# Kernel tuning notes

Hardware: AMD Instinct MI355X
Metric: run time of the kernel (lower is better)

The kernel has to match this reference:

```python
import jax, jax.numpy as jnp
import numpy as np

K = 3          # kernel_size
STRIDE = 1
PAD = 1
DIL = 1


def setup_inputs() -> dict:
    key = jax.random.key(0)
    k1, k2, k3, k4, k5 = jax.random.split(key, 5)
    x = jax.random.normal(k1, (4, 64, 128, 128), jnp.float32)
    weight = jax.random.normal(k2, (64, 64, K, K), jnp.float32) * 0.05   # [O, C, K, K]
    bias = jax.random.normal(k3, (64,), jnp.float32) * 0.05
    # offset conv params: small nonzero so offsets actually exercise bilinear sampling
    offset_w = jax.random.normal(k4, (2 * K * K, 64, K, K), jnp.float32) * 0.01
    offset_b = jax.random.normal(k5, (2 * K * K,), jnp.float32) * 0.1
    return {"x": x, "weight": weight, "bias": bias,
            "offset_w": offset_w, "offset_b": offset_b}


def _conv2d(x, w, b):
    y = jax.lax.conv_general_dilated(
        x, w, window_strides=(STRIDE, STRIDE),
        padding=((PAD, PAD), (PAD, PAD)), rhs_dilation=(DIL, DIL),
        dimension_numbers=("NCHW", "OIHW", "NCHW"))
    return y + b[None, :, None, None]


def _bilinear_sample(img, ys, xs):
    # img: [C, H, W]; ys, xs: [KK, Ho, Wo] float sampling coords
    H, W = img.shape[1], img.shape[2]
    y0 = jnp.floor(ys)
    x0 = jnp.floor(xs)
    y1 = y0 + 1.0
    x1 = x0 + 1.0
    wy1 = ys - y0
    wx1 = xs - x0
    wy0 = 1.0 - wy1
    wx0 = 1.0 - wx1

    def gather(yy, xx):
        valid = (yy >= 0) & (yy <= H - 1) & (xx >= 0) & (xx <= W - 1)
        yi = jnp.clip(yy, 0, H - 1).astype(jnp.int32)
        xi = jnp.clip(xx, 0, W - 1).astype(jnp.int32)
        v = img[:, yi, xi]                     # [C, KK, Ho, Wo]
        return v * valid.astype(img.dtype)

    return (gather(y0, x0) * (wy0 * wx0) + gather(y0, x1) * (wy0 * wx1)
            + gather(y1, x0) * (wy1 * wx0) + gather(y1, x1) * (wy1 * wx1))


def reference(x, weight, bias, offset_w, offset_b):
    B, C, H, W = x.shape
    KK = K * K
    # offsets: [B, 2*K*K, Ho, Wo], per-location (dy, dx) for each kernel tap
    offset = _conv2d(x, offset_w, offset_b)
    Ho, Wo = offset.shape[2], offset.shape[3]
    off = offset.reshape(B, KK, 2, Ho, Wo)
    dy, dx = off[:, :, 0], off[:, :, 1]        # [B, KK, Ho, Wo]

    ki, kj = jnp.meshgrid(jnp.arange(K), jnp.arange(K), indexing="ij")
    ki = ki.reshape(KK).astype(x.dtype)
    kj = kj.reshape(KK).astype(x.dtype)
    oy = (jnp.arange(Ho) * STRIDE - PAD).astype(x.dtype)
    ox = (jnp.arange(Wo) * STRIDE - PAD).astype(x.dtype)
    base_y = oy[None, :, None] + (ki * DIL)[:, None, None]   # [KK, Ho, 1]
    base_x = ox[None, None, :] + (kj * DIL)[:, None, None]   # [KK, 1, Wo]
    ys = base_y[None] + dy                                   # [B, KK, Ho, Wo]
    xs = base_x[None] + dx

    # sampled: [B, C, KK, Ho, Wo]
    sampled = jax.vmap(_bilinear_sample)(x, ys, xs)
    w = weight.reshape(weight.shape[0], C, KK)
    out = jnp.einsum("bckhw,ock->bohw", sampled, w) + bias[None, :, None, None]
    return out
```

## Files before the change

### kernel.cpp

```cpp
#include <hip/hip_runtime.h>
#include <hip/hip_bf16.h>

#define B_ 4
#define C_ 64
#define H_ 128
#define W_ 128
#define HW_ (H_ * W_)
#define OCH_ 18

typedef __attribute__((ext_vector_type(8))) short short8;
typedef __attribute__((ext_vector_type(16))) float f32x16;
typedef __attribute__((ext_vector_type(2))) float float2v;

#define W2B_ELEMS (9 * 2 * 4 * 64 * 8)
#define W2A_ELEMS (36 * 64 * 8)

#define PSTRIDE_B (6 * 128 * 16 + 16)
#define WIN_BYTES (8 * PSTRIDE_B)
#define OFFL_OFS  WIN_BYTES
#define OFFW_B    (OCH_ * 32 * 4)
#define SMEM_BYTES (WIN_BYTES + 8 * OFFW_B)

__device__ __forceinline__ unsigned short f2bf(float f) {
  union { float f; unsigned u; } v; v.f = f;
  unsigned r = v.u + 0x7FFFu + ((v.u >> 16) & 1u);
  return (unsigned short)(r >> 16);
}
__device__ __forceinline__ float bf2f(unsigned short h) {
  union { unsigned u; float f; } v; v.u = ((unsigned)h) << 16;
  return v.f;
}
__device__ __forceinline__ unsigned short f2bfh(float f) {
  __hip_bfloat16 h = __float2bfloat16(f);
  return *reinterpret_cast<unsigned short*>(&h);
}
__device__ __forceinline__ float uaf(unsigned u) {
  union { unsigned u; float f; } v; v.u = u; return v.f;
}
__device__ __forceinline__ int swz256(int x) { return (x & 7) * 32 + (x >> 3); }

__global__ __launch_bounds__(256) void pack_w_only(
    const float* __restrict__ wmain, const float* __restrict__ offw,
    unsigned short* __restrict__ ws_u) {
  int idx = blockIdx.x * 256 + threadIdx.x;
  if (idx < W2B_ELEMS) {
    int i = idx & 7, lane = (idx >> 3) & 63, s = (idx >> 9) & 3;
    int mq = (idx >> 11) & 1, t = idx >> 12;
    int o = mq * 32 + (lane & 31);
    int c = 16 * s + (lane >> 5) * 8 + i;
    ws_u[idx] = f2bf(wmain[(o * 64 + c) * 9 + t]);
  } else if (idx < W2B_ELEMS + W2A_ELEMS) {
    int j = idx - W2B_ELEMS;
    int i = j & 7, lane = (j >> 3) & 63, s = j >> 9;
    int kg = 16 * s + (lane >> 5) * 8 + i;
    int t = kg >> 6, c = kg & 63, oc = lane & 31;
    ws_u[idx] = (oc < OCH_) ? f2bf(offw[(oc * 64 + c) * 9 + t]) : (unsigned short)0;
  }
}

__global__ __launch_bounds__(512, 2) void deform_fused8(
    const float* __restrict__ x, const float* __restrict__ bias,
    const float* __restrict__ ob, const unsigned short* __restrict__ w2b,
    const unsigned short* __restrict__ w2a, float* __restrict__ out) {
  const int blk = swz256(blockIdx.x);
  const int ho0 = (blk & 63) * 2;
  const int b   = blk >> 6;
  const int tid = threadIdx.x;
  const int lane = tid & 63;
  const int wave = tid >> 6;
  const int r_off = wave >> 2;
  const int pair  = wave & 3;
  const int ho = ho0 + r_off;
  const int pxl = lane & 31;
  const int px = pair * 32 + pxl;
  const int laneh = lane >> 5;

  __shared__ __align__(16) char smem[SMEM_BYTES];

  const float* xb = x + (size_t)b * C_ * HW_;
  #pragma unroll
  for (int it = 0; it < 3; ++it) {
    const int u = tid + it * 512;
    const int row  = u >> 8;
    const int p    = (u >> 5) & 7;
    const int col4 = u & 31;
    const int srow = min(H_ - 1, max(0, ho0 - 2 + row));
    const float* bp = xb + (size_t)(p * 8) * HW_ + srow * W_ + col4 * 4;
    float4 f[8];
    #pragma unroll
    for (int i = 0; i < 8; ++i) f[i] = *(const float4*)(bp + (size_t)i * HW_);
    char* outb = smem + p * PSTRIDE_B + (((row << 7) + col4 * 4) << 4);
    #pragma unroll
    for (int j = 0; j < 4; ++j) {
      short8 v;
      #pragma unroll
      for (int i = 0; i < 8; ++i)
        v[i] = (short)f2bfh(reinterpret_cast<const float*>(&f[i])[j]);
      *(short8*)(outb + j * 16) = v;
    }
  }
  __syncthreads();

  f32x16 pacc_a, pacc_b;
  #pragma unroll
  for (int r = 0; r < 16; ++r) { pacc_a[r] = 0.f; pacc_b[r] = 0.f; }

  #pragma unroll 1
  for (int sq = 0; sq < 18; ++sq) {
    #pragma unroll
    for (int h = 0; h < 2; ++h) {
      const int s = 2 * sq + h;
      const int t = s >> 2;
      const int ki = (t >= 6) ? 2 : ((t >= 3) ? 1 : 0);
      const int kj = t - 3 * ki;
      const int row = ho - 1 + ki;
      const int col = px - 1 + kj;
      short8 bfr = {0, 0, 0, 0, 0, 0, 0, 0};
      if (((unsigned)row < (unsigned)H_) && ((unsigned)col < (unsigned)W_))
        bfr = *(const short8*)(smem + ((s & 3) * 2 + laneh) * PSTRIDE_B
                               + ((((ki + 1 + r_off) << 7) + col) << 4));
      const short8 afr = *(const short8*)&w2a[((size_t)s * 64 + lane) * 8];
      if (h)
        pacc_b = __builtin_amdgcn_mfma_f32_32x32x16_bf16(afr, bfr, pacc_b, 0, 0, 0);
      else
        pacc_a = __builtin_amdgcn_mfma_f32_32x32x16_bf16(afr, bfr, pacc_a, 0, 0, 0);
    }
  }

  float* offl = (float*)(smem + OFFL_OFS + wave * OFFW_B);
  #pragma unroll
  for (int reg = 0; reg < 16; ++reg) {
    const int oc = (reg & 3) + 8 * (reg >> 2) + 4 * laneh;
    if (oc < OCH_) offl[oc * 32 + pxl] = pacc_a[reg] + pacc_b[reg] + ob[oc];
  }

  f32x16 acc0, acc1;
  #pragma unroll
  for (int r = 0; r < 16; ++r) { acc0[r] = 0.f; acc1[r] = 0.f; }

  #pragma unroll 1
  for (int t = 0; t < 9; ++t) {
    const int ki = (t >= 6) ? 2 : ((t >= 3) ? 1 : 0);
    const int kj = t - 3 * ki;
    const float dy = offl[(2 * t) * 32 + pxl];
    const float dx = offl[(2 * t + 1) * 32 + pxl];
    const float ys = (float)(ho - 1 + ki) + dy;
    const float xs = (float)(px - 1 + kj) + dx;
    const float y0f = floorf(ys), x0f = floorf(xs);
    const int y0 = (int)y0f, x0 = (int)x0f;
    const int y1 = y0 + 1, x1 = x0 + 1;
    const float wy1 = ys - y0f, wx1 = xs - x0f;
    const float wy0 = 1.f - wy1, wx0 = 1.f - wx1;
    const bool vy0 = (unsigned)y0 < (unsigned)H_, vy1 = (unsigned)y1 < (unsigned)H_;
    const bool vx0 = (unsigned)x0 < (unsigned)W_, vx1 = (unsigned)x1 < (unsigned)W_;
    const float g00 = (vy0 && vx0) ? wy0 * wx0 : 0.f;
    const float g01 = (vy0 && vx1) ? wy0 * wx1 : 0.f;
    const float g10 = (vy1 && vx0) ? wy1 * wx0 : 0.f;
    const float g11 = (vy1 && vx1) ? wy1 * wx1 : 0.f;
    const int yc0 = min(max(y0, 0), H_ - 1), yc1 = min(max(y1, 0), H_ - 1);
    const int xc0 = min(max(x0, 0), W_ - 1), xc1 = min(max(x1, 0), W_ - 1);
    const int rr0 = yc0 - ho0 + 2, rr1 = yc1 - ho0 + 2;
    const bool in = ((unsigned)rr0 < 6u) & ((unsigned)rr1 < 6u);
    const unsigned short* wt2 = w2b + t * 4096;

    if (__builtin_expect(__any(!in), 0)) {
      #pragma unroll 1
      for (int ss = 0; ss < 4; ++ss) {
        short8 bf;
        #pragma unroll
        for (int i = 0; i < 8; ++i) {
          const float* img = xb + (size_t)((2 * ss + laneh) * 8 + i) * HW_;
          float v = g00 * img[yc0 * W_ + xc0] + g01 * img[yc0 * W_ + xc1]
                  + g10 * img[yc1 * W_ + xc0] + g11 * img[yc1 * W_ + xc1];
          bf[i] = (short)f2bfh(v);
        }
        const short8 a0 = *(const short8*)&wt2[(ss * 64 + lane) * 8];
        const short8 a1 = *(const short8*)&wt2[((4 + ss) * 64 + lane) * 8];
        acc0 = __builtin_amdgcn_mfma_f32_32x32x16_bf16(a0, bf, acc0, 0, 0, 0);
        acc1 = __builtin_amdgcn_mfma_f32_32x32x16_bf16(a1, bf, acc1, 0, 0, 0);
      }
      continue;
    }

    const int u00 = ((rr0 << 7) + xc0) << 4, u01 = ((rr0 << 7) + xc1) << 4;
    const int u10 = ((rr1 << 7) + xc0) << 4, u11 = ((rr1 << 7) + xc1) << 4;

    short8 c00[4], c01[4], c10[4], c11[4];
    #pragma unroll
    for (int ss = 0; ss < 4; ++ss) {
      const char* pb = smem + (2 * ss + laneh) * PSTRIDE_B;
      c00[ss] = *(const short8*)(pb + u00);
      c01[ss] = *(const short8*)(pb + u01);
      c10[ss] = *(const short8*)(pb + u10);
      c11[ss] = *(const short8*)(pb + u11);
    }

    #pragma unroll
    for (int ss = 0; ss < 4; ++ss) {
      short8 bf;
      #pragma unroll
      for (int d = 0; d < 4; ++d) {
        const unsigned w00 = ((const unsigned*)&c00[ss])[d];
        const unsigned w01 = ((const unsigned*)&c01[ss])[d];
        const unsigned w10 = ((const unsigned*)&c10[ss])[d];
        const unsigned w11 = ((const unsigned*)&c11[ss])[d];
        float2v p00, p01, p10, p11;
        p00.x = uaf(w00 << 16); p00.y = uaf(w00 & 0xFFFF0000u);
        p01.x = uaf(w01 << 16); p01.y = uaf(w01 & 0xFFFF0000u);
        p10.x = uaf(w10 << 16); p10.y = uaf(w10 & 0xFFFF0000u);
        p11.x = uaf(w11 << 16); p11.y = uaf(w11 & 0xFFFF0000u);
        float2v v = p00 * g00 + p01 * g01 + p10 * g10 + p11 * g11;
        ((unsigned*)&bf)[d] = (unsigned)f2bfh(v.x) | ((unsigned)f2bfh(v.y) << 16);
      }
      const short8 a0 = *(const short8*)&wt2[(ss * 64 + lane) * 8];
      const short8 a1 = *(const short8*)&wt2[((4 + ss) * 64 + lane) * 8];
      acc0 = __builtin_amdgcn_mfma_f32_32x32x16_bf16(a0, bf, acc0, 0, 0, 0);
      acc1 = __builtin_amdgcn_mfma_f32_32x32x16_bf16(a1, bf, acc1, 0, 0, 0);
    }
  }

  #pragma unroll
  for (int reg = 0; reg < 16; ++reg) {
    const int row = (reg & 3) + 8 * (reg >> 2) + 4 * laneh;
    out[((b * 64 + row)      * H_ + ho) * W_ + px] = acc0[reg] + bias[row];
    out[((b * 64 + 32 + row) * H_ + ho) * W_ + px] = acc1[reg] + bias[32 + row];
  }
}

extern "C" void kernel_launch(void* const* d_in, const int* in_sizes, int n_in,
                              void* d_out, int out_size, void* d_ws, size_t ws_size,
                              hipStream_t stream) {
  const float* x    = (const float*)d_in[0];
  const float* wt   = (const float*)d_in[1];
  const float* bias = (const float*)d_in[2];
  const float* ow   = (const float*)d_in[3];
  const float* ob   = (const float*)d_in[4];
  float* out = (float*)d_out;

  unsigned short* ws_u = (unsigned short*)d_ws;
  unsigned short* w2b  = ws_u;
  unsigned short* w2a  = ws_u + W2B_ELEMS;

  const int pack_blocks = (W2B_ELEMS + W2A_ELEMS + 255) / 256;
  pack_w_only<<<pack_blocks, 256, 0, stream>>>(wt, ow, ws_u);

  deform_fused8<<<B_ * (H_ / 2), 512, 0, stream>>>(x, bias, ob, w2b, w2a, out);
}
```

Measured before the change: 41.87 us.

## Switch to fp16 with packed bilinear math, swizzled LDS, unrolled taps, split fallback

```diff
diff --git a/kernel.cpp b/kernel.cpp
--- a/kernel.cpp
+++ b/kernel.cpp
@@ -8,9 +8,9 @@
 #define HW_ (H_ * W_)
 #define OCH_ 18
 
-typedef __attribute__((ext_vector_type(8))) short short8;
-typedef __attribute__((ext_vector_type(16))) float f32x16;
-typedef __attribute__((ext_vector_type(2))) float float2v;
+typedef __attribute__((ext_vector_type(2)))  _Float16 half2v;
+typedef __attribute__((ext_vector_type(8)))  _Float16 half8;
+typedef __attribute__((ext_vector_type(16))) float    f32x16;
 
 #define W2B_ELEMS (9 * 2 * 4 * 64 * 8)
 #define W2A_ELEMS (36 * 64 * 8)
@@ -21,23 +21,18 @@
 #define OFFW_B    (OCH_ * 32 * 4)
 #define SMEM_BYTES (WIN_BYTES + 8 * OFFW_B)
 
-__device__ __forceinline__ unsigned short f2bf(float f) {
-  union { float f; unsigned u; } v; v.f = f;
-  unsigned r = v.u + 0x7FFFu + ((v.u >> 16) & 1u);
-  return (unsigned short)(r >> 16);
-}
-__device__ __forceinline__ float bf2f(unsigned short h) {
-  union { unsigned u; float f; } v; v.u = ((unsigned)h) << 16;
-  return v.f;
-}
-__device__ __forceinline__ unsigned short f2bfh(float f) {
-  __hip_bfloat16 h = __float2bfloat16(f);
+__device__ __forceinline__ unsigned short f2h(float f) {
+  _Float16 h = (_Float16)f;
   return *reinterpret_cast<unsigned short*>(&h);
 }
-__device__ __forceinline__ float uaf(unsigned u) {
-  union { unsigned u; float f; } v; v.u = u; return v.f;
+__device__ __forceinline__ half2v pkrtz(float a, float b) {
+  auto p = __builtin_amdgcn_cvt_pkrtz(a, b);
+  return *reinterpret_cast<half2v*>(&p);
 }
 __device__ __forceinline__ int swz256(int x) { return (x & 7) * 32 + (x >> 3); }
+__device__ __forceinline__ int SWU(int row, int col) {
+  return (((row << 7) + (col & ~3) + ((col & 3) ^ ((col >> 3) & 3))) << 4);
+}
 
 __global__ __launch_bounds__(256) void pack_w_only(
     const float* __restrict__ wmain, const float* __restrict__ offw,
@@ -48,17 +43,78 @@
     int mq = (idx >> 11) & 1, t = idx >> 12;
     int o = mq * 32 + (lane & 31);
     int c = 16 * s + (lane >> 5) * 8 + i;
-    ws_u[idx] = f2bf(wmain[(o * 64 + c) * 9 + t]);
+    ws_u[idx] = f2h(wmain[(o * 64 + c) * 9 + t]);
   } else if (idx < W2B_ELEMS + W2A_ELEMS) {
     int j = idx - W2B_ELEMS;
     int i = j & 7, lane = (j >> 3) & 63, s = j >> 9;
     int kg = 16 * s + (lane >> 5) * 8 + i;
     int t = kg >> 6, c = kg & 63, oc = lane & 31;
-    ws_u[idx] = (oc < OCH_) ? f2bf(offw[(oc * 64 + c) * 9 + t]) : (unsigned short)0;
-  }
-}
-
-__global__ __launch_bounds__(512, 2) void deform_fused8(
+    ws_u[idx] = (oc < OCH_) ? f2h(offw[(oc * 64 + c) * 9 + t]) : (unsigned short)0;
+  }
+}
+
+template<int T>
+__device__ __forceinline__ void tap_fast(
+    const float* __restrict__ offl, int pxl, int ho, int ho0, int px,
+    int lane, int laneh, const char* __restrict__ smem,
+    const unsigned short* __restrict__ w2b,
+    f32x16& acc0, f32x16& acc1, unsigned& fm) {
+  constexpr int KI = T / 3, KJ = T - 3 * (T / 3);
+  const float dy = offl[(2 * T) * 32 + pxl];
+  const float dx = offl[(2 * T + 1) * 32 + pxl];
+  const float ys = (float)(ho - 1 + KI) + dy;
+  const float xs = (float)(px - 1 + KJ) + dx;
+  const float y0f = floorf(ys), x0f = floorf(xs);
+  const int y0 = (int)y0f, x0 = (int)x0f;
+  const int y1 = y0 + 1, x1 = x0 + 1;
+  const float wy1 = ys - y0f, wx1 = xs - x0f;
+  const float wy0 = 1.f - wy1, wx0 = 1.f - wx1;
+  const bool vy0 = (unsigned)y0 < (unsigned)H_, vy1 = (unsigned)y1 < (unsigned)H_;
+  const bool vx0 = (unsigned)x0 < (unsigned)W_, vx1 = (unsigned)x1 < (unsigned)W_;
+  const float g00 = (vy0 && vx0) ? wy0 * wx0 : 0.f;
+  const float g01 = (vy0 && vx1) ? wy0 * wx1 : 0.f;
+  const float g10 = (vy1 && vx0) ? wy1 * wx0 : 0.f;
+  const float g11 = (vy1 && vx1) ? wy1 * wx1 : 0.f;
+  const int yc0 = min(max(y0, 0), H_ - 1), yc1 = min(max(y1, 0), H_ - 1);
+  const int xc0 = min(max(x0, 0), W_ - 1), xc1 = min(max(x1, 0), W_ - 1);
+  const int rr0 = yc0 - ho0 + 2, rr1 = yc1 - ho0 + 2;
+  const bool wr0 = (unsigned)rr0 < 6u, wr1 = (unsigned)rr1 < 6u;
+  const float gg00 = wr0 ? g00 : 0.f, gg01 = wr0 ? g01 : 0.f;
+  const float gg10 = wr1 ? g10 : 0.f, gg11 = wr1 ? g11 : 0.f;
+  if (__any((!wr0 & (vy0 & (vx0 | vx1))) | (!wr1 & (vy1 & (vx0 | vx1)))))
+    fm |= (1u << T);
+  const int cr0 = min(max(rr0, 0), 5), cr1 = min(max(rr1, 0), 5);
+  const int u00 = SWU(cr0, xc0), u01 = SWU(cr0, xc1);
+  const int u10 = SWU(cr1, xc0), u11 = SWU(cr1, xc1);
+  half2v G00; G00.x = G00.y = (_Float16)gg00;
+  half2v G01; G01.x = G01.y = (_Float16)gg01;
+  half2v G10; G10.x = G10.y = (_Float16)gg10;
+  half2v G11; G11.x = G11.y = (_Float16)gg11;
+  const unsigned short* wt2 = w2b + T * 4096;
+
+  #pragma unroll
+  for (int ss = 0; ss < 4; ++ss) {
+    const char* pb = smem + (2 * ss + laneh) * PSTRIDE_B;
+    const half8 c00 = *(const half8*)(pb + u00);
+    const half8 c01 = *(const half8*)(pb + u01);
+    const half8 c10 = *(const half8*)(pb + u10);
+    const half8 c11 = *(const half8*)(pb + u11);
+    const half2v* p00 = (const half2v*)&c00;
+    const half2v* p01 = (const half2v*)&c01;
+    const half2v* p10 = (const half2v*)&c10;
+    const half2v* p11 = (const half2v*)&c11;
+    union { half8 v; half2v h[4]; } bf;
+    #pragma unroll
+    for (int d = 0; d < 4; ++d)
+      bf.h[d] = p00[d] * G00 + p01[d] * G01 + p10[d] * G10 + p11[d] * G11;
+    const half8 a0 = *(const half8*)&wt2[(ss * 64 + lane) * 8];
+    const half8 a1 = *(const half8*)&wt2[((4 + ss) * 64 + lane) * 8];
+    acc0 = __builtin_amdgcn_mfma_f32_32x32x16_f16(a0, bf.v, acc0, 0, 0, 0);
+    acc1 = __builtin_amdgcn_mfma_f32_32x32x16_f16(a1, bf.v, acc1, 0, 0, 0);
+  }
+}
+
+__global__ __launch_bounds__(512, 2) void deform_fused9(
     const float* __restrict__ x, const float* __restrict__ bias,
     const float* __restrict__ ob, const unsigned short* __restrict__ w2b,
     const unsigned short* __restrict__ w2a, float* __restrict__ out) {
@@ -89,14 +145,15 @@
     float4 f[8];
     #pragma unroll
     for (int i = 0; i < 8; ++i) f[i] = *(const float4*)(bp + (size_t)i * HW_);
-    char* outb = smem + p * PSTRIDE_B + (((row << 7) + col4 * 4) << 4);
+    char* outb = smem + p * PSTRIDE_B;
     #pragma unroll
     for (int j = 0; j < 4; ++j) {
-      short8 v;
+      union { half8 v; half2v h[4]; } o;
       #pragma unroll
-      for (int i = 0; i < 8; ++i)
-        v[i] = (short)f2bfh(reinterpret_cast<const float*>(&f[i])[j]);
-      *(short8*)(outb + j * 16) = v;
+      for (int k = 0; k < 4; ++k)
+        o.h[k] = pkrtz(reinterpret_cast<const float*>(&f[2 * k])[j],
+                       reinterpret_cast<const float*>(&f[2 * k + 1])[j]);
+      *(half8*)(outb + SWU(row, col4 * 4 + j)) = o.v;
     }
   }
   __syncthreads();
@@ -115,15 +172,15 @@
       const int kj = t - 3 * ki;
       const int row = ho - 1 + ki;
       const int col = px - 1 + kj;
-      short8 bfr = {0, 0, 0, 0, 0, 0, 0, 0};
+      half8 bfr = {0, 0, 0, 0, 0, 0, 0, 0};
       if (((unsigned)row < (unsigned)H_) && ((unsigned)col < (unsigned)W_))
-        bfr = *(const short8*)(smem + ((s & 3) * 2 + laneh) * PSTRIDE_B
-                               + ((((ki + 1 + r_off) << 7) + col) << 4));
-      const short8 afr = *(const short8*)&w2a[((size_t)s * 64 + lane) * 8];
+        bfr = *(const half8*)(smem + ((s & 3) * 2 + laneh) * PSTRIDE_B
+                              + SWU(ki + 1 + r_off, col));
+      const half8 afr = *(const half8*)&w2a[((size_t)s * 64 + lane) * 8];
       if (h)
-        pacc_b = __builtin_amdgcn_mfma_f32_32x32x16_bf16(afr, bfr, pacc_b, 0, 0, 0);
+        pacc_b = __builtin_amdgcn_mfma_f32_32x32x16_f16(afr, bfr, pacc_b, 0, 0, 0);
       else
-        pacc_a = __builtin_amdgcn_mfma_f32_32x32x16_bf16(afr, bfr, pacc_a, 0, 0, 0);
+        pacc_a = __builtin_amdgcn_mfma_f32_32x32x16_f16(afr, bfr, pacc_a, 0, 0, 0);
     }
   }
 
@@ -137,85 +194,61 @@
   f32x16 acc0, acc1;
   #pragma unroll
   for (int r = 0; r < 16; ++r) { acc0[r] = 0.f; acc1[r] = 0.f; }
-
-  #pragma unroll 1
-  for (int t = 0; t < 9; ++t) {
-    const int ki = (t >= 6) ? 2 : ((t >= 3) ? 1 : 0);
-    const int kj = t - 3 * ki;
-    const float dy = offl[(2 * t) * 32 + pxl];
-    const float dx = offl[(2 * t + 1) * 32 + pxl];
-    const float ys = (float)(ho - 1 + ki) + dy;
-    const float xs = (float)(px - 1 + kj) + dx;
-    const float y0f = floorf(ys), x0f = floorf(xs);
-    const int y0 = (int)y0f, x0 = (int)x0f;
-    const int y1 = y0 + 1, x1 = x0 + 1;
-    const float wy1 = ys - y0f, wx1 = xs - x0f;
-    const float wy0 = 1.f - wy1, wx0 = 1.f - wx1;
-    const bool vy0 = (unsigned)y0 < (unsigned)H_, vy1 = (unsigned)y1 < (unsigned)H_;
-    const bool vx0 = (unsigned)x0 < (unsigned)W_, vx1 = (unsigned)x1 < (unsigned)W_;
-    const float g00 = (vy0 && vx0) ? wy0 * wx0 : 0.f;
-    const float g01 = (vy0 && vx1) ? wy0 * wx1 : 0.f;
-    const float g10 = (vy1 && vx0) ? wy1 * wx0 : 0.f;
-    const float g11 = (vy1 && vx1) ? wy1 * wx1 : 0.f;
-    const int yc0 = min(max(y0, 0), H_ - 1), yc1 = min(max(y1, 0), H_ - 1);
-    const int xc0 = min(max(x0, 0), W_ - 1), xc1 = min(max(x1, 0), W_ - 1);
-    const int rr0 = yc0 - ho0 + 2, rr1 = yc1 - ho0 + 2;
-    const bool in = ((unsigned)rr0 < 6u) & ((unsigned)rr1 < 6u);
-    const unsigned short* wt2 = w2b + t * 4096;
-
-    if (__builtin_expect(__any(!in), 0)) {
+  unsigned fm = 0;
+
+  tap_fast<0>(offl, pxl, ho, ho0, px, lane, laneh, smem, w2b, acc0, acc1, fm);
+  tap_fast<1>(offl, pxl, ho, ho0, px, lane, laneh, smem, w2b, acc0, acc1, fm);
+  tap_fast<2>(offl, pxl, ho, ho0, px, lane, laneh, smem, w2b, acc0, acc1, fm);
+  tap_fast<3>(offl, pxl, ho, ho0, px, lane, laneh, smem, w2b, acc0, acc1, fm);
+  tap_fast<4>(offl, pxl, ho, ho0, px, lane, laneh, smem, w2b, acc0, acc1, fm);
+  tap_fast<5>(offl, pxl, ho, ho0, px, lane, laneh, smem, w2b, acc0, acc1, fm);
+  tap_fast<6>(offl, pxl, ho, ho0, px, lane, laneh, smem, w2b, acc0, acc1, fm);
+  tap_fast<7>(offl, pxl, ho, ho0, px, lane, laneh, smem, w2b, acc0, acc1, fm);
+  tap_fast<8>(offl, pxl, ho, ho0, px, lane, laneh, smem, w2b, acc0, acc1, fm);
+
+  if (__builtin_expect(fm != 0, 0)) {
+    #pragma unroll 1
+    for (int t = 0; t < 9; ++t) {
+      if (!((fm >> t) & 1)) continue;
+      const int ki = (t >= 6) ? 2 : ((t >= 3) ? 1 : 0);
+      const int kj = t - 3 * ki;
+      const float dy = offl[(2 * t) * 32 + pxl];
+      const float dx = offl[(2 * t + 1) * 32 + pxl];
+      const float ys = (float)(ho - 1 + ki) + dy;
+      const float xs = (float)(px - 1 + kj) + dx;
+      const float y0f = floorf(ys), x0f = floorf(xs);
+      const int y0 = (int)y0f, x0 = (int)x0f;
+      const int y1 = y0 + 1, x1 = x0 + 1;
+      const float wy1 = ys - y0f, wx1 = xs - x0f;
+      const float wy0 = 1.f - wy1, wx0 = 1.f - wx1;
+      const bool vy0 = (unsigned)y0 < (unsigned)H_, vy1 = (unsigned)y1 < (unsigned)H_;
+      const bool vx0 = (unsigned)x0 < (unsigned)W_, vx1 = (unsigned)x1 < (unsigned)W_;
+      float g00 = (vy0 && vx0) ? wy0 * wx0 : 0.f;
+      float g01 = (vy0 && vx1) ? wy0 * wx1 : 0.f;
+      float g10 = (vy1 && vx0) ? wy1 * wx0 : 0.f;
+      float g11 = (vy1 && vx1) ? wy1 * wx1 : 0.f;
+      const int yc0 = min(max(y0, 0), H_ - 1), yc1 = min(max(y1, 0), H_ - 1);
+      const int xc0 = min(max(x0, 0), W_ - 1), xc1 = min(max(x1, 0), W_ - 1);
+      const bool wr0 = (unsigned)(yc0 - ho0 + 2) < 6u;
+      const bool wr1 = (unsigned)(yc1 - ho0 + 2) < 6u;
+      g00 = wr0 ? 0.f : g00; g01 = wr0 ? 0.f : g01;
+      g10 = wr1 ? 0.f : g10; g11 = wr1 ? 0.f : g11;
+      const unsigned short* wt2 = w2b + t * 4096;
       #pragma unroll 1
       for (int ss = 0; ss < 4; ++ss) {
-        short8 bf;
+        union { half8 v; _Float16 e[8]; } bf;
         #pragma unroll
         for (int i = 0; i < 8; ++i) {
           const float* img = xb + (size_t)((2 * ss + laneh) * 8 + i) * HW_;
           float v = g00 * img[yc0 * W_ + xc0] + g01 * img[yc0 * W_ + xc1]
                   + g10 * img[yc1 * W_ + xc0] + g11 * img[yc1 * W_ + xc1];
-          bf[i] = (short)f2bfh(v);
+          bf.e[i] = (_Float16)v;
         }
-        const short8 a0 = *(const short8*)&wt2[(ss * 64 + lane) * 8];
-        const short8 a1 = *(const short8*)&wt2[((4 + ss) * 64 + lane) * 8];
-        acc0 = __builtin_amdgcn_mfma_f32_32x32x16_bf16(a0, bf, acc0, 0, 0, 0);
-        acc1 = __builtin_amdgcn_mfma_f32_32x32x16_bf16(a1, bf, acc1, 0, 0, 0);
+        const half8 a0 = *(const half8*)&wt2[(ss * 64 + lane) * 8];
+        const half8 a1 = *(const half8*)&wt2[((4 + ss) * 64 + lane) * 8];
+        acc0 = __builtin_amdgcn_mfma_f32_32x32x16_f16(a0, bf.v, acc0, 0, 0, 0);
+        acc1 = __builtin_amdgcn_mfma_f32_32x32x16_f16(a1, bf.v, acc1, 0, 0, 0);
       }
-      continue;
-    }
-
-    const int u00 = ((rr0 << 7) + xc0) << 4, u01 = ((rr0 << 7) + xc1) << 4;
-    const int u10 = ((rr1 << 7) + xc0) << 4, u11 = ((rr1 << 7) + xc1) << 4;
-
-    short8 c00[4], c01[4], c10[4], c11[4];
-    #pragma unroll
-    for (int ss = 0; ss < 4; ++ss) {
-      const char* pb = smem + (2 * ss + laneh) * PSTRIDE_B;
-      c00[ss] = *(const short8*)(pb + u00);
-      c01[ss] = *(const short8*)(pb + u01);
-      c10[ss] = *(const short8*)(pb + u10);
-      c11[ss] = *(const short8*)(pb + u11);
-    }
-
-    #pragma unroll
-    for (int ss = 0; ss < 4; ++ss) {
-      short8 bf;
-      #pragma unroll
-      for (int d = 0; d < 4; ++d) {
-        const unsigned w00 = ((const unsigned*)&c00[ss])[d];
-        const unsigned w01 = ((const unsigned*)&c01[ss])[d];
-        const unsigned w10 = ((const unsigned*)&c10[ss])[d];
-        const unsigned w11 = ((const unsigned*)&c11[ss])[d];
-        float2v p00, p01, p10, p11;
-        p00.x = uaf(w00 << 16); p00.y = uaf(w00 & 0xFFFF0000u);
-        p01.x = uaf(w01 << 16); p01.y = uaf(w01 & 0xFFFF0000u);
-        p10.x = uaf(w10 << 16); p10.y = uaf(w10 & 0xFFFF0000u);
-        p11.x = uaf(w11 << 16); p11.y = uaf(w11 & 0xFFFF0000u);
-        float2v v = p00 * g00 + p01 * g01 + p10 * g10 + p11 * g11;
-        ((unsigned*)&bf)[d] = (unsigned)f2bfh(v.x) | ((unsigned)f2bfh(v.y) << 16);
-      }
-      const short8 a0 = *(const short8*)&wt2[(ss * 64 + lane) * 8];
-      const short8 a1 = *(const short8*)&wt2[((4 + ss) * 64 + lane) * 8];
-      acc0 = __builtin_amdgcn_mfma_f32_32x32x16_bf16(a0, bf, acc0, 0, 0, 0);
-      acc1 = __builtin_amdgcn_mfma_f32_32x32x16_bf16(a1, bf, acc1, 0, 0, 0);
     }
   }
 
@@ -244,5 +277,5 @@
   const int pack_blocks = (W2B_ELEMS + W2A_ELEMS + 255) / 256;
   pack_w_only<<<pack_blocks, 256, 0, stream>>>(wt, ow, ws_u);
 
-  deform_fused8<<<B_ * (H_ / 2), 512, 0, stream>>>(x, bias, ob, w2b, w2a, out);
-}
+  deform_fused9<<<B_ * (H_ / 2), 512, 0, stream>>>(x, bias, ob, w2b, w2a, out);
+}
```

New measurement: 36.90 us. 1.13x faster.
